# Kernel tuning notes

Measured on AMD Instinct MI355X. Metric: run time of the kernel, lower is better.

## Reference

```python
import jax, jax.numpy as jnp
import numpy as np

N_NODES = 50000
N_EDGES = 625000
F_IN = 128
HIDDEN = 128
N_CLASSES = 64


def setup_inputs() -> dict:
    key = jax.random.key(0)
    ks = jax.random.split(key, 8)
    x = jax.random.normal(ks[0], (N_NODES, F_IN), dtype=jnp.float32)
    edge_index = jax.random.randint(ks[1], (2, N_EDGES), 0, N_NODES, dtype=jnp.int64)
    # GCNConv weights (glorot-ish scale) and biases
    def glorot(k, fan_in, fan_out):
        s = jnp.sqrt(6.0 / (fan_in + fan_out))
        return jax.random.uniform(k, (fan_in, fan_out), minval=-s, maxval=s, dtype=jnp.float32)
    W1 = glorot(ks[2], F_IN, HIDDEN)
    b1 = jnp.zeros((HIDDEN,), dtype=jnp.float32)
    W2 = glorot(ks[3], HIDDEN, HIDDEN)
    b2 = jnp.zeros((HIDDEN,), dtype=jnp.float32)
    Wf = glorot(ks[4], HIDDEN, N_CLASSES)
    bf = jnp.zeros((N_CLASSES,), dtype=jnp.float32)
    return {"x": x, "edge_index": edge_index, "W1": W1, "b1": b1,
            "W2": W2, "b2": b2, "Wf": Wf, "bf": bf}


def reference(x, edge_index, W1, b1, W2, b2, Wf, bf):
    # Inference mode: AdaptiveDropout and F.dropout are identity (training=False).
    N = x.shape[0]
    loop = jnp.arange(N, dtype=edge_index.dtype)
    src = jnp.concatenate([edge_index[0], loop])  # source nodes (with self-loops)
    dst = jnp.concatenate([edge_index[1], loop])  # target nodes (with self-loops)
    # Symmetric GCN normalization: deg from edge weights scattered to targets
    deg = jax.ops.segment_sum(jnp.ones(dst.shape[0], dtype=x.dtype), dst, num_segments=N)
    dinv = jnp.where(deg > 0, jax.lax.rsqrt(deg), 0.0)
    norm = dinv[src] * dinv[dst]  # [E+N]

    def gcn(h, W, b):
        m = h @ W                      # [N, out]
        msg = m[src] * norm[:, None]   # gather + scale  [E+N, out]
        return jax.ops.segment_sum(msg, dst, num_segments=N) + b

    h = jax.nn.relu(gcn(x, W1, b1))
    h = jax.nn.relu(gcn(h, W2, b2))
    logits = gcn(h, Wf, bf)
    return jax.nn.log_softmax(logits, axis=1)
```

## Files before the change

### kernel.cpp

```cpp
#include <hip/hip_runtime.h>
#include <cstdint>
#include <cstddef>


#define WAVE 64
typedef _Float16 f16;
typedef f16  f16x2 __attribute__((ext_vector_type(2)));
typedef f16  f16x4 __attribute__((ext_vector_type(4)));
typedef f16  f16x8 __attribute__((ext_vector_type(8)));
typedef float f32x4 __attribute__((ext_vector_type(4)));


__global__ void k_zero(int4* __restrict__ p, int n4) {
    int i = blockIdx.x * blockDim.x + threadIdx.x;
    if (i < n4) p[i] = make_int4(0, 0, 0, 0);
}

__global__ void k_count(const int* __restrict__ dst, int E, int* __restrict__ cnt, int N) {
    int e = blockIdx.x * blockDim.x + threadIdx.x;
    if (e >= E) return;
    int d = dst[e];
    if (d >= 0 && d < N) atomicAdd(&cnt[d], 1);
}

__global__ __launch_bounds__(256) void k_blocksum(const int* __restrict__ cnt, int N,
                                                  int* __restrict__ partial) {
    const int t  = threadIdx.x;
    const int b  = blockIdx.x;
    const int i0 = b * 1024 + t * 4;
    int s = 0;
#pragma unroll
    for (int j = 0; j < 4; ++j) {
        int i = i0 + j;
        if (i < N) s += cnt[i];
    }
#pragma unroll
    for (int o = 32; o > 0; o >>= 1) s += __shfl_xor(s, o);
    __shared__ int ws[4];
    if ((t & 63) == 0) ws[t >> 6] = s;
    __syncthreads();
    if (t == 0) partial[b] = ws[0] + ws[1] + ws[2] + ws[3];
}

__global__ __launch_bounds__(256) void k_blockscan(const int* __restrict__ cnt, int N,
                                                   const int* __restrict__ partial, int numB,
                                                   int* __restrict__ offs,
                                                   float* __restrict__ dinv,
                                                   int* __restrict__ cursor) {
    const int t  = threadIdx.x;
    const int b  = blockIdx.x;
    const int i0 = b * 1024 + t * 4;
    __shared__ int sbase;
    __shared__ int ws[4];

    if (t < 64) {
        int v = 0;
        for (int i = t; i < b; i += 64) v += partial[i];
#pragma unroll
        for (int o = 32; o > 0; o >>= 1) v += __shfl_xor(v, o);
        if (t == 0) sbase = v;
    }

    int c[4];
    int tsum = 0;
#pragma unroll
    for (int j = 0; j < 4; ++j) {
        int i = i0 + j;
        c[j] = (i < N) ? cnt[i] : 0;
        tsum += c[j];
    }
    int incl = tsum;
#pragma unroll
    for (int o = 1; o < 64; o <<= 1) {
        int u = __shfl_up(incl, o);
        if ((t & 63) >= o) incl += u;
    }
    const int wid = t >> 6;
    if ((t & 63) == 63) ws[wid] = incl;
    __syncthreads();
    int wbase = 0;
    for (int w = 0; w < wid; ++w) wbase += ws[w];
    int run = sbase + wbase + (incl - tsum);
#pragma unroll
    for (int j = 0; j < 4; ++j) {
        int i = i0 + j;
        if (i < N) {
            offs[i]   = run;
            run      += c[j];
            dinv[i]   = rsqrtf((float)(c[j] + 1));
            cursor[i] = 0;
        }
    }
    if (b == numB - 1 && t == 0)
        offs[N] = sbase + ws[0] + ws[1] + ws[2] + ws[3];
}

__global__ void k_scatter(const int* __restrict__ src, const int* __restrict__ dst, int E,
                          const int* __restrict__ offsets, int* __restrict__ cursor,
                          int* __restrict__ src_s, int N) {
    int e = blockIdx.x * blockDim.x + threadIdx.x;
    if (e >= E) return;
    int d = dst[e], s = src[e];
    if (d < 0 || d >= N || s < 0 || s >= N) return;
    int p = offsets[d] + atomicAdd(&cursor[d], 1);
    src_s[p] = s;
}

__global__ void k_cvt_w_all(const float* __restrict__ W1, const float* __restrict__ W2,
                            const float* __restrict__ Wf,
                            f16* __restrict__ Wt1, f16* __restrict__ Wt2,
                            f16* __restrict__ Wtf) {
    int i = blockIdx.x * 256 + threadIdx.x;
    if (i < 16384) {
        int n = i >> 7, k = i & 127;
        Wt1[i] = (f16)W1[k * 128 + n];
    } else if (i < 32768) {
        int j = i - 16384;
        int n = j >> 7, k = j & 127;
        Wt2[j] = (f16)W2[k * 128 + n];
    } else if (i < 40960) {
        int j = i - 32768;
        int n = j >> 7, k = j & 127;
        Wtf[j] = (f16)Wf[k * 64 + n];
    }
}

template <int OUT, bool AF32>
__global__ __launch_bounds__(256) void k_gemm_mfma(const void* __restrict__ Av,
                                                   const f16* __restrict__ Wt,
                                                   const float* __restrict__ dinv,
                                                   f16* __restrict__ M,
                                                   int N) {
    constexpr int K  = 128;
    constexpr int CW = OUT / 64;
    __shared__ char smem[OUT * K * 2];
    __shared__ float dl[64];

    const int t    = threadIdx.x;
    const int w    = t >> 6;
    const int lane = t & 63;
    const int ln   = lane & 15;
    const int lh   = lane >> 4;
    const int row0 = blockIdx.x * 64;

    {
        constexpr int NCH = OUT * 16;
        for (int j = t; j < NCH; j += 256) {
            int n = j >> 4;
            uint32_t byte = (uint32_t)j * 16;
            uint32_t swz  = byte ^ (uint32_t)((n & 7) << 4);
            *(f16x8*)(smem + swz) = *(const f16x8*)&Wt[(size_t)j * 8];
        }
        if (t < 64) {
            int r = row0 + t;
            dl[t] = dinv[r < N ? r : (N - 1)];
        }
    }
    __syncthreads();

    f16x8 bfr[CW][4];
    const int c0 = w * CW;
#pragma unroll
    for (int c = 0; c < CW; ++c) {
        int n = (c0 + c) * 16 + ln;
#pragma unroll
        for (int q = 0; q < 4; ++q) {
            uint32_t byte = (uint32_t)(n * 256 + q * 64 + lh * 16);
            uint32_t swz  = byte ^ (uint32_t)((n & 7) << 4);
            bfr[c][q] = *(const f16x8*)(smem + swz);
        }
    }
    __syncthreads();

    f32x4 acc[4][CW];
#pragma unroll
    for (int s = 0; s < 4; ++s)
#pragma unroll
        for (int c = 0; c < CW; ++c)
            acc[s][c] = f32x4{0.f, 0.f, 0.f, 0.f};

#pragma unroll
    for (int s = 0; s < 4; ++s) {
        int m = row0 + s * 16 + ln;
        const size_t mrow = (size_t)(m < N ? m : (N - 1)) * K;
#pragma unroll
        for (int q = 0; q < 4; ++q) {
            f16x8 a;
            if constexpr (AF32) {
                const float* ap = (const float*)Av + mrow + q * 32 + lh * 8;
                float4 x0 = *(const float4*)ap;
                float4 x1 = *(const float4*)(ap + 4);
                a = f16x8{ (f16)x0.x, (f16)x0.y, (f16)x0.z, (f16)x0.w,
                           (f16)x1.x, (f16)x1.y, (f16)x1.z, (f16)x1.w };
            } else {
                a = *(const f16x8*)((const f16*)Av + mrow + q * 32 + lh * 8);
            }
#pragma unroll
            for (int c = 0; c < CW; ++c)
                acc[s][c] = __builtin_amdgcn_mfma_f32_16x16x32_f16(a, bfr[c][q], acc[s][c], 0, 0, 0);
        }
    }

    f16* ot = (f16*)smem;
#pragma unroll
    for (int s = 0; s < 4; ++s) {
#pragma unroll
        for (int c = 0; c < CW; ++c) {
            int col = (c0 + c) * 16 + ln;
#pragma unroll
            for (int r = 0; r < 4; ++r) {
                int rl = s * 16 + lh * 4 + r;
                ot[rl * OUT + col] = (f16)(acc[s][c][r] * dl[rl]);
            }
        }
    }
    __syncthreads();

    constexpr int CPR = OUT / 8;
    for (int j = t; j < 64 * CPR; j += 256) {
        int rl = j / CPR;
        if (row0 + rl < N)
            *(f16x8*)&M[(size_t)(row0 + rl) * OUT + (j % CPR) * 8] =
                *(const f16x8*)&ot[(size_t)j * 8];
    }
}

__global__ __launch_bounds__(256) void k_agg128_f16(const f16* __restrict__ M16,
                                                    const int* __restrict__ offs,
                                                    const int* __restrict__ srcs,
                                                    const float* __restrict__ dinv,
                                                    const float* __restrict__ bias,
                                                    f16* __restrict__ H16, int N) {
    const int lane = threadIdx.x & (WAVE - 1);
    const int sub  = lane >> 5;
    const int hl   = lane & 31;
    const int q    = hl >> 4;
    const int fl   = lane & 15;
    const int fo   = fl * 8;
    const int node = blockIdx.x * 8 + (threadIdx.x >> 6) * 2 + sub;
    if (node >= N) return;

    float a[8] = {0.f, 0.f, 0.f, 0.f, 0.f, 0.f, 0.f, 0.f};
    if (q == 0) {
        f16x8 v = *(const f16x8*)&M16[(size_t)node * 128 + fo];
#pragma unroll
        for (int i = 0; i < 8; ++i) a[i] = (float)v[i];
    }

    const int e0 = offs[node], e1 = offs[node + 1];
    for (int base = e0; base < e1; base += 16) {
        int   s[8];
        float w[8];
#pragma unroll
        for (int j = 0; j < 8; ++j) {
            int i = base + 2 * j + q;
            bool ok = i < e1;
            s[j] = srcs[ok ? i : e0];
            w[j] = ok ? 1.f : 0.f;
        }
        f16x8 v[8];
#pragma unroll
        for (int j = 0; j < 8; ++j)
            v[j] = *(const f16x8*)&M16[(size_t)s[j] * 128 + fo];
#pragma unroll
        for (int j = 0; j < 8; ++j)
#pragma unroll
            for (int i = 0; i < 8; ++i)
                a[i] += w[j] * (float)v[j][i];
    }

#pragma unroll
    for (int i = 0; i < 8; ++i) a[i] += __shfl_xor(a[i], 16);

    if (q == 0) {
        const float dn = dinv[node];
        float4 b0 = *(const float4*)&bias[fo];
        float4 b1 = *(const float4*)&bias[fo + 4];
        f16x8 o;
        o[0] = (f16)fmaxf(a[0] * dn + b0.x, 0.f);
        o[1] = (f16)fmaxf(a[1] * dn + b0.y, 0.f);
        o[2] = (f16)fmaxf(a[2] * dn + b0.z, 0.f);
        o[3] = (f16)fmaxf(a[3] * dn + b0.w, 0.f);
        o[4] = (f16)fmaxf(a[4] * dn + b1.x, 0.f);
        o[5] = (f16)fmaxf(a[5] * dn + b1.y, 0.f);
        o[6] = (f16)fmaxf(a[6] * dn + b1.z, 0.f);
        o[7] = (f16)fmaxf(a[7] * dn + b1.w, 0.f);
        *(f16x8*)&H16[(size_t)node * 128 + fo] = o;
    }
}

__global__ __launch_bounds__(256) void k_agg64_lsm(const f16* __restrict__ M16,
                                                   const int* __restrict__ offs,
                                                   const int* __restrict__ srcs,
                                                   const float* __restrict__ dinv,
                                                   const float* __restrict__ bias,
                                                   float* __restrict__ Y, int N) {
    const int lane = threadIdx.x & (WAVE - 1);
    const int sub  = lane >> 5;
    const int hl   = lane & 31;
    const int q    = hl >> 4;
    const int fl   = lane & 15;
    const int fo   = fl * 4;
    const int node = blockIdx.x * 8 + (threadIdx.x >> 6) * 2 + sub;
    if (node >= N) return;

    float a[4] = {0.f, 0.f, 0.f, 0.f};
    if (q == 0) {
        f16x4 v = *(const f16x4*)&M16[(size_t)node * 64 + fo];
#pragma unroll
        for (int i = 0; i < 4; ++i) a[i] = (float)v[i];
    }

    const int e0 = offs[node], e1 = offs[node + 1];
    for (int base = e0; base < e1; base += 16) {
        int   s[8];
        float w[8];
#pragma unroll
        for (int j = 0; j < 8; ++j) {
            int i = base + 2 * j + q;
            bool ok = i < e1;
            s[j] = srcs[ok ? i : e0];
            w[j] = ok ? 1.f : 0.f;
        }
        f16x4 v[8];
#pragma unroll
        for (int j = 0; j < 8; ++j)
            v[j] = *(const f16x4*)&M16[(size_t)s[j] * 64 + fo];
#pragma unroll
        for (int j = 0; j < 8; ++j)
#pragma unroll
            for (int i = 0; i < 4; ++i)
                a[i] += w[j] * (float)v[j][i];
    }

#pragma unroll
    for (int i = 0; i < 4; ++i) a[i] += __shfl_xor(a[i], 16);

    const float dn = dinv[node];
    float4 b = *(const float4*)&bias[fo];
    float v0 = a[0] * dn + b.x;
    float v1 = a[1] * dn + b.y;
    float v2 = a[2] * dn + b.z;
    float v3 = a[3] * dn + b.w;
    float m = fmaxf(fmaxf(v0, v1), fmaxf(v2, v3));
#pragma unroll
    for (int o = 8; o > 0; o >>= 1) m = fmaxf(m, __shfl_xor(m, o));
    float s = expf(v0 - m) + expf(v1 - m) + expf(v2 - m) + expf(v3 - m);
#pragma unroll
    for (int o = 8; o > 0; o >>= 1) s += __shfl_xor(s, o);
    if (q == 0) {
        float ls = logf(s);
        float4 o4 = make_float4(v0 - m - ls, v1 - m - ls, v2 - m - ls, v3 - m - ls);
        *(float4*)&Y[(size_t)node * 64 + fo] = o4;
    }
}


extern "C" void kernel_launch(void* const* d_in, const int* in_sizes, int n_in,
                              void* d_out, int out_size, void* d_ws, size_t ws_size,
                              hipStream_t stream) {
    const float* x  = (const float*)d_in[0];
    const int*   ei = (const int*)d_in[1];
    const float* W1 = (const float*)d_in[2];
    const float* b1 = (const float*)d_in[3];
    const float* W2 = (const float*)d_in[4];
    const float* b2 = (const float*)d_in[5];
    const float* Wf = (const float*)d_in[6];
    const float* bf = (const float*)d_in[7];
    float* out = (float*)d_out;

    const int N = in_sizes[0] / 128;
    const int E = in_sizes[1] / 2;
    const int* src = ei;
    const int* dst = ei + E;

    char* ws = (char*)d_ws;
    auto alloc = [&](size_t bytes) -> void* {
        void* p = ws;
        ws += (bytes + 255) & ~(size_t)255;
        return p;
    };
    const int numB = (N + 1023) / 1024;
    int*   cnt    = (int*)alloc((size_t)N * 4);
    int*   cursor = (int*)alloc((size_t)N * 4);
    int*   offs   = (int*)alloc((size_t)(N + 1) * 4);
    float* dinv   = (float*)alloc((size_t)N * 4);
    int*   part   = (int*)alloc((size_t)numB * 4);
    int*   src_s  = (int*)alloc((size_t)E * 4);
    f16*   m16    = (f16*)alloc((size_t)N * 128 * 2);
    f16*   h16    = (f16*)alloc((size_t)N * 128 * 2);
    f16*   Wt1    = (f16*)alloc(128 * 128 * 2);
    f16*   Wt2    = (f16*)alloc(128 * 128 * 2);
    f16*   Wtf    = (f16*)alloc(128 * 64 * 2);

    const int TB = 256;
    const int n4 = (N + 3) / 4;
    k_zero<<<(n4 + TB - 1) / TB, TB, 0, stream>>>((int4*)cnt, n4);
    k_count<<<(E + TB - 1) / TB, TB, 0, stream>>>(dst, E, cnt, N);
    k_blocksum<<<numB, 256, 0, stream>>>(cnt, N, part);
    k_blockscan<<<numB, 256, 0, stream>>>(cnt, N, part, numB, offs, dinv, cursor);
    k_scatter<<<(E + TB - 1) / TB, TB, 0, stream>>>(src, dst, E, offs, cursor, src_s, N);
    k_cvt_w_all<<<160, 256, 0, stream>>>(W1, W2, Wf, Wt1, Wt2, Wtf);

    const int gemm_grid = (N + 63) / 64;
    const int agg_grid  = (N + 7) / 8;

    k_gemm_mfma<128, true><<<gemm_grid, 256, 0, stream>>>(x, Wt1, dinv, m16, N);
    k_agg128_f16<<<agg_grid, 256, 0, stream>>>(m16, offs, src_s, dinv, b1, h16, N);

    k_gemm_mfma<128, false><<<gemm_grid, 256, 0, stream>>>(h16, Wt2, dinv, m16, N);
    k_agg128_f16<<<agg_grid, 256, 0, stream>>>(m16, offs, src_s, dinv, b2, h16, N);

    k_gemm_mfma<64, false><<<gemm_grid, 256, 0, stream>>>(h16, Wtf, dinv, m16, N);
    k_agg64_lsm<<<agg_grid, 256, 0, stream>>>(m16, offs, src_s, dinv, bf, out, N);
}
```

Before: 201.2 us.

## Fuse whole GCN pipeline into one cooperative persistent kernel with grid syncs

Replaces the twelve separate launches (CSR build, weight conversion, three GEMM and aggregation pairs) with a single cooperative persistent kernel that loops over tiles and separates phases with grid.sync(). It also overlaps the edge scatter with the first GEMM in the same phase. The aim is to remove per-launch overhead and tail gaps between small kernels. In exchange, occupancy is capped by the cooperative-launch limit and the 32KB static shared memory, and every grid barrier stalls the whole device. The old multi-kernel path stays as a fallback if the cooperative launch fails.

```diff
diff --git a/kernel.cpp b/kernel.cpp
--- a/kernel.cpp
+++ b/kernel.cpp
@@ -1,6 +1,9 @@
 #include <hip/hip_runtime.h>
+#include <hip/hip_cooperative_groups.h>
 #include <cstdint>
 #include <cstddef>
+
+namespace cg = cooperative_groups;
 
 
 #define WAVE 64
@@ -11,106 +14,10 @@
 typedef float f32x4 __attribute__((ext_vector_type(4)));
 
 
-__global__ void k_zero(int4* __restrict__ p, int n4) {
-    int i = blockIdx.x * blockDim.x + threadIdx.x;
-    if (i < n4) p[i] = make_int4(0, 0, 0, 0);
-}
-
-__global__ void k_count(const int* __restrict__ dst, int E, int* __restrict__ cnt, int N) {
-    int e = blockIdx.x * blockDim.x + threadIdx.x;
-    if (e >= E) return;
-    int d = dst[e];
-    if (d >= 0 && d < N) atomicAdd(&cnt[d], 1);
-}
-
-__global__ __launch_bounds__(256) void k_blocksum(const int* __restrict__ cnt, int N,
-                                                  int* __restrict__ partial) {
-    const int t  = threadIdx.x;
-    const int b  = blockIdx.x;
-    const int i0 = b * 1024 + t * 4;
-    int s = 0;
-#pragma unroll
-    for (int j = 0; j < 4; ++j) {
-        int i = i0 + j;
-        if (i < N) s += cnt[i];
-    }
-#pragma unroll
-    for (int o = 32; o > 0; o >>= 1) s += __shfl_xor(s, o);
-    __shared__ int ws[4];
-    if ((t & 63) == 0) ws[t >> 6] = s;
-    __syncthreads();
-    if (t == 0) partial[b] = ws[0] + ws[1] + ws[2] + ws[3];
-}
-
-__global__ __launch_bounds__(256) void k_blockscan(const int* __restrict__ cnt, int N,
-                                                   const int* __restrict__ partial, int numB,
-                                                   int* __restrict__ offs,
-                                                   float* __restrict__ dinv,
-                                                   int* __restrict__ cursor) {
-    const int t  = threadIdx.x;
-    const int b  = blockIdx.x;
-    const int i0 = b * 1024 + t * 4;
-    __shared__ int sbase;
-    __shared__ int ws[4];
-
-    if (t < 64) {
-        int v = 0;
-        for (int i = t; i < b; i += 64) v += partial[i];
-#pragma unroll
-        for (int o = 32; o > 0; o >>= 1) v += __shfl_xor(v, o);
-        if (t == 0) sbase = v;
-    }
-
-    int c[4];
-    int tsum = 0;
-#pragma unroll
-    for (int j = 0; j < 4; ++j) {
-        int i = i0 + j;
-        c[j] = (i < N) ? cnt[i] : 0;
-        tsum += c[j];
-    }
-    int incl = tsum;
-#pragma unroll
-    for (int o = 1; o < 64; o <<= 1) {
-        int u = __shfl_up(incl, o);
-        if ((t & 63) >= o) incl += u;
-    }
-    const int wid = t >> 6;
-    if ((t & 63) == 63) ws[wid] = incl;
-    __syncthreads();
-    int wbase = 0;
-    for (int w = 0; w < wid; ++w) wbase += ws[w];
-    int run = sbase + wbase + (incl - tsum);
-#pragma unroll
-    for (int j = 0; j < 4; ++j) {
-        int i = i0 + j;
-        if (i < N) {
-            offs[i]   = run;
-            run      += c[j];
-            dinv[i]   = rsqrtf((float)(c[j] + 1));
-            cursor[i] = 0;
-        }
-    }
-    if (b == numB - 1 && t == 0)
-        offs[N] = sbase + ws[0] + ws[1] + ws[2] + ws[3];
-}
-
-__global__ void k_scatter(const int* __restrict__ src, const int* __restrict__ dst, int E,
-                          const int* __restrict__ offsets, int* __restrict__ cursor,
-                          int* __restrict__ src_s, int N) {
-    int e = blockIdx.x * blockDim.x + threadIdx.x;
-    if (e >= E) return;
-    int d = dst[e], s = src[e];
-    if (d < 0 || d >= N || s < 0 || s >= N) return;
-    int p = offsets[d] + atomicAdd(&cursor[d], 1);
-    src_s[p] = s;
-}
-
-__global__ void k_cvt_w_all(const float* __restrict__ W1, const float* __restrict__ W2,
-                            const float* __restrict__ Wf,
-                            f16* __restrict__ Wt1, f16* __restrict__ Wt2,
-                            f16* __restrict__ Wtf) {
-    int i = blockIdx.x * 256 + threadIdx.x;
+__device__ __forceinline__ void cvtw_elem(int i,
+    const float* __restrict__ W1, const float* __restrict__ W2,
+    const float* __restrict__ Wf,
+    f16* __restrict__ Wt1, f16* __restrict__ Wt2, f16* __restrict__ Wtf) {
     if (i < 16384) {
         int n = i >> 7, k = i & 127;
         Wt1[i] = (f16)W1[k * 128 + n];
@@ -125,23 +32,86 @@
     }
 }
 
+__device__ __forceinline__ void blocksum_body(const int* __restrict__ cnt, int N,
+                                              int* __restrict__ part, int b, int t,
+                                              int* ws4) {
+    const int i0 = b * 1024 + t * 4;
+    int s = 0;
+#pragma unroll
+    for (int j = 0; j < 4; ++j) {
+        int i = i0 + j;
+        if (i < N) s += cnt[i];
+    }
+#pragma unroll
+    for (int o = 32; o > 0; o >>= 1) s += __shfl_xor(s, o);
+    if ((t & 63) == 0) ws4[t >> 6] = s;
+    __syncthreads();
+    if (t == 0) part[b] = ws4[0] + ws4[1] + ws4[2] + ws4[3];
+    __syncthreads();
+}
+
+__device__ __forceinline__ void blockscan_body(const int* __restrict__ cnt, int N,
+                                               const int* __restrict__ part, int numB,
+                                               int* __restrict__ offs,
+                                               float* __restrict__ dinv,
+                                               int* __restrict__ cursor,
+                                               int b, int t, int* ws4, int* sbase) {
+    const int i0 = b * 1024 + t * 4;
+    if (t < 64) {
+        int v = 0;
+        for (int i = t; i < b; i += 64) v += part[i];
+#pragma unroll
+        for (int o = 32; o > 0; o >>= 1) v += __shfl_xor(v, o);
+        if (t == 0) *sbase = v;
+    }
+    int c[4];
+    int tsum = 0;
+#pragma unroll
+    for (int j = 0; j < 4; ++j) {
+        int i = i0 + j;
+        c[j] = (i < N) ? cnt[i] : 0;
+        tsum += c[j];
+    }
+    int incl = tsum;
+#pragma unroll
+    for (int o = 1; o < 64; o <<= 1) {
+        int u = __shfl_up(incl, o);
+        if ((t & 63) >= o) incl += u;
+    }
+    const int wid = t >> 6;
+    if ((t & 63) == 63) ws4[wid] = incl;
+    __syncthreads();
+    int wbase = 0;
+    for (int w = 0; w < wid; ++w) wbase += ws4[w];
+    int run = *sbase + wbase + (incl - tsum);
+#pragma unroll
+    for (int j = 0; j < 4; ++j) {
+        int i = i0 + j;
+        if (i < N) {
+            offs[i]   = run;
+            run      += c[j];
+            dinv[i]   = rsqrtf((float)(c[j] + 1));
+            cursor[i] = 0;
+        }
+    }
+    if (b == numB - 1 && t == 0)
+        offs[N] = *sbase + ws4[0] + ws4[1] + ws4[2] + ws4[3];
+    __syncthreads();
+}
+
 template <int OUT, bool AF32>
-__global__ __launch_bounds__(256) void k_gemm_mfma(const void* __restrict__ Av,
-                                                   const f16* __restrict__ Wt,
-                                                   const float* __restrict__ dinv,
-                                                   f16* __restrict__ M,
-                                                   int N) {
+__device__ __forceinline__ void gemm_tile(const void* __restrict__ Av,
+                                          const f16* __restrict__ Wt,
+                                          const float* __restrict__ dinv,
+                                          f16* __restrict__ M, int N, int row0,
+                                          char* smem, float* dl) {
     constexpr int K  = 128;
     constexpr int CW = OUT / 64;
-    __shared__ char smem[OUT * K * 2];
-    __shared__ float dl[64];
-
     const int t    = threadIdx.x;
     const int w    = t >> 6;
     const int lane = t & 63;
     const int ln   = lane & 15;
     const int lh   = lane >> 4;
-    const int row0 = blockIdx.x * 64;
 
     {
         constexpr int NCH = OUT * 16;
@@ -223,21 +193,22 @@
             *(f16x8*)&M[(size_t)(row0 + rl) * OUT + (j % CPR) * 8] =
                 *(const f16x8*)&ot[(size_t)j * 8];
     }
-}
-
-__global__ __launch_bounds__(256) void k_agg128_f16(const f16* __restrict__ M16,
-                                                    const int* __restrict__ offs,
-                                                    const int* __restrict__ srcs,
-                                                    const float* __restrict__ dinv,
-                                                    const float* __restrict__ bias,
-                                                    f16* __restrict__ H16, int N) {
-    const int lane = threadIdx.x & (WAVE - 1);
+    __syncthreads();
+}
+
+__device__ __forceinline__ void agg128_tile(const f16* __restrict__ M16,
+                                            const int* __restrict__ offs,
+                                            const int* __restrict__ srcs,
+                                            const float* __restrict__ dinv,
+                                            const float* __restrict__ bias,
+                                            f16* __restrict__ H16, int N, int vb) {
+    const int t    = threadIdx.x;
+    const int lane = t & (WAVE - 1);
     const int sub  = lane >> 5;
-    const int hl   = lane & 31;
-    const int q    = hl >> 4;
+    const int q    = (lane & 31) >> 4;
     const int fl   = lane & 15;
     const int fo   = fl * 8;
-    const int node = blockIdx.x * 8 + (threadIdx.x >> 6) * 2 + sub;
+    const int node = vb * 8 + (t >> 6) * 2 + sub;
     if (node >= N) return;
 
     float a[8] = {0.f, 0.f, 0.f, 0.f, 0.f, 0.f, 0.f, 0.f};
@@ -289,19 +260,19 @@
     }
 }
 
-__global__ __launch_bounds__(256) void k_agg64_lsm(const f16* __restrict__ M16,
-                                                   const int* __restrict__ offs,
-                                                   const int* __restrict__ srcs,
-                                                   const float* __restrict__ dinv,
-                                                   const float* __restrict__ bias,
-                                                   float* __restrict__ Y, int N) {
-    const int lane = threadIdx.x & (WAVE - 1);
+__device__ __forceinline__ void agg64_tile(const f16* __restrict__ M16,
+                                           const int* __restrict__ offs,
+                                           const int* __restrict__ srcs,
+                                           const float* __restrict__ dinv,
+                                           const float* __restrict__ bias,
+                                           float* __restrict__ Y, int N, int vb) {
+    const int t    = threadIdx.x;
+    const int lane = t & (WAVE - 1);
     const int sub  = lane >> 5;
-    const int hl   = lane & 31;
-    const int q    = hl >> 4;
+    const int q    = (lane & 31) >> 4;
     const int fl   = lane & 15;
     const int fo   = fl * 4;
-    const int node = blockIdx.x * 8 + (threadIdx.x >> 6) * 2 + sub;
+    const int node = vb * 8 + (t >> 6) * 2 + sub;
     if (node >= N) return;
 
     float a[4] = {0.f, 0.f, 0.f, 0.f};
@@ -353,6 +324,173 @@
         float4 o4 = make_float4(v0 - m - ls, v1 - m - ls, v2 - m - ls, v3 - m - ls);
         *(float4*)&Y[(size_t)node * 64 + fo] = o4;
     }
+}
+
+
+__global__ __launch_bounds__(256, 4) void k_mega(
+    const float* __restrict__ x, const int* __restrict__ srcv, const int* __restrict__ dstv,
+    const float* __restrict__ W1, const float* __restrict__ b1,
+    const float* __restrict__ W2, const float* __restrict__ b2,
+    const float* __restrict__ Wf, const float* __restrict__ bf,
+    float* __restrict__ out,
+    int* cnt, int* cursor, int* offs, float* dinv, int* part, int* src_s,
+    f16* m16, f16* h16, f16* Wt1, f16* Wt2, f16* Wtf,
+    int N, int E, int numB) {
+    cg::grid_group grid = cg::this_grid();
+    __shared__ char  smem[32768];
+    __shared__ float dl[64];
+    __shared__ int   ws4[4];
+    __shared__ int   sbase;
+
+    const int t    = threadIdx.x;
+    const int gtid = blockIdx.x * 256 + t;
+    const int gsz  = gridDim.x * 256;
+
+    {
+        const int n4 = (N + 3) >> 2;
+        const int4 z = make_int4(0, 0, 0, 0);
+        for (int i = gtid; i < n4; i += gsz) ((int4*)cnt)[i] = z;
+        for (int i = gtid; i < 40960; i += gsz) cvtw_elem(i, W1, W2, Wf, Wt1, Wt2, Wtf);
+    }
+    grid.sync();
+
+    for (int e = gtid; e < E; e += gsz) {
+        int d = dstv[e];
+        if ((unsigned)d < (unsigned)N) atomicAdd(&cnt[d], 1);
+    }
+    grid.sync();
+
+    for (int b = blockIdx.x; b < numB; b += gridDim.x)
+        blocksum_body(cnt, N, part, b, t, ws4);
+    grid.sync();
+
+    for (int b = blockIdx.x; b < numB; b += gridDim.x)
+        blockscan_body(cnt, N, part, numB, offs, dinv, cursor, b, t, ws4, &sbase);
+    grid.sync();
+
+    for (int e = gtid; e < E; e += gsz) {
+        int d = dstv[e], s = srcv[e];
+        if ((unsigned)d < (unsigned)N && (unsigned)s < (unsigned)N) {
+            int p = offs[d] + atomicAdd(&cursor[d], 1);
+            src_s[p] = s;
+        }
+    }
+    {
+        const int tiles = (N + 63) >> 6;
+        for (int vt = blockIdx.x; vt < tiles; vt += gridDim.x)
+            gemm_tile<128, true>(x, Wt1, dinv, m16, N, vt * 64, smem, dl);
+    }
+    grid.sync();
+
+    {
+        const int vbs = (N + 7) >> 3;
+        for (int vb = blockIdx.x; vb < vbs; vb += gridDim.x)
+            agg128_tile(m16, offs, src_s, dinv, b1, h16, N, vb);
+    }
+    grid.sync();
+
+    {
+        const int tiles = (N + 63) >> 6;
+        for (int vt = blockIdx.x; vt < tiles; vt += gridDim.x)
+            gemm_tile<128, false>(h16, Wt2, dinv, m16, N, vt * 64, smem, dl);
+    }
+    grid.sync();
+
+    {
+        const int vbs = (N + 7) >> 3;
+        for (int vb = blockIdx.x; vb < vbs; vb += gridDim.x)
+            agg128_tile(m16, offs, src_s, dinv, b2, h16, N, vb);
+    }
+    grid.sync();
+
+    {
+        const int tiles = (N + 63) >> 6;
+        for (int vt = blockIdx.x; vt < tiles; vt += gridDim.x)
+            gemm_tile<64, false>(h16, Wtf, dinv, m16, N, vt * 64, smem, dl);
+    }
+    grid.sync();
+
+    {
+        const int vbs = (N + 7) >> 3;
+        for (int vb = blockIdx.x; vb < vbs; vb += gridDim.x)
+            agg64_tile(m16, offs, src_s, dinv, bf, out, N, vb);
+    }
+}
+
+
+__global__ void k_zero(int4* __restrict__ p, int n4) {
+    int i = blockIdx.x * blockDim.x + threadIdx.x;
+    if (i < n4) p[i] = make_int4(0, 0, 0, 0);
+}
+
+__global__ void k_count(const int* __restrict__ dst, int E, int* __restrict__ cnt, int N) {
+    int e = blockIdx.x * blockDim.x + threadIdx.x;
+    if (e >= E) return;
+    int d = dst[e];
+    if ((unsigned)d < (unsigned)N) atomicAdd(&cnt[d], 1);
+}
+
+__global__ __launch_bounds__(256) void k_blocksum(const int* __restrict__ cnt, int N,
+                                                  int* __restrict__ part) {
+    __shared__ int ws4[4];
+    blocksum_body(cnt, N, part, blockIdx.x, threadIdx.x, ws4);
+}
+
+__global__ __launch_bounds__(256) void k_blockscan(const int* __restrict__ cnt, int N,
+                                                   const int* __restrict__ part, int numB,
+                                                   int* __restrict__ offs,
+                                                   float* __restrict__ dinv,
+                                                   int* __restrict__ cursor) {
+    __shared__ int ws4[4];
+    __shared__ int sbase;
+    blockscan_body(cnt, N, part, numB, offs, dinv, cursor, blockIdx.x, threadIdx.x, ws4, &sbase);
+}
+
+__global__ void k_scatter(const int* __restrict__ src, const int* __restrict__ dst, int E,
+                          const int* __restrict__ offsets, int* __restrict__ cursor,
+                          int* __restrict__ src_s, int N) {
+    int e = blockIdx.x * blockDim.x + threadIdx.x;
+    if (e >= E) return;
+    int d = dst[e], s = src[e];
+    if ((unsigned)d >= (unsigned)N || (unsigned)s >= (unsigned)N) return;
+    int p = offsets[d] + atomicAdd(&cursor[d], 1);
+    src_s[p] = s;
+}
+
+__global__ void k_cvt_w_all(const float* __restrict__ W1, const float* __restrict__ W2,
+                            const float* __restrict__ Wf,
+                            f16* __restrict__ Wt1, f16* __restrict__ Wt2,
+                            f16* __restrict__ Wtf) {
+    int i = blockIdx.x * 256 + threadIdx.x;
+    cvtw_elem(i, W1, W2, Wf, Wt1, Wt2, Wtf);
+}
+
+template <int OUT, bool AF32>
+__global__ __launch_bounds__(256) void k_gemm_mfma(const void* __restrict__ Av,
+                                                   const f16* __restrict__ Wt,
+                                                   const float* __restrict__ dinv,
+                                                   f16* __restrict__ M, int N) {
+    __shared__ char  smem[OUT * 128 * 2];
+    __shared__ float dl[64];
+    gemm_tile<OUT, AF32>(Av, Wt, dinv, M, N, blockIdx.x * 64, smem, dl);
+}
+
+__global__ __launch_bounds__(256) void k_agg128_f16(const f16* __restrict__ M16,
+                                                    const int* __restrict__ offs,
+                                                    const int* __restrict__ srcs,
+                                                    const float* __restrict__ dinv,
+                                                    const float* __restrict__ bias,
+                                                    f16* __restrict__ H16, int N) {
+    agg128_tile(M16, offs, srcs, dinv, bias, H16, N, blockIdx.x);
+}
+
+__global__ __launch_bounds__(256) void k_agg64_lsm(const f16* __restrict__ M16,
+                                                   const int* __restrict__ offs,
+                                                   const int* __restrict__ srcs,
+                                                   const float* __restrict__ dinv,
+                                                   const float* __restrict__ bias,
+                                                   float* __restrict__ Y, int N) {
+    agg64_tile(M16, offs, srcs, dinv, bias, Y, N, blockIdx.x);
 }
 
 
@@ -371,8 +509,8 @@
 
     const int N = in_sizes[0] / 128;
     const int E = in_sizes[1] / 2;
-    const int* src = ei;
-    const int* dst = ei + E;
+    const int* srcv = ei;
+    const int* dstv = ei + E;
 
     char* ws = (char*)d_ws;
     auto alloc = [&](size_t bytes) -> void* {
@@ -381,7 +519,7 @@
         return p;
     };
     const int numB = (N + 1023) / 1024;
-    int*   cnt    = (int*)alloc((size_t)N * 4);
+    int*   cnt    = (int*)alloc((size_t)N * 4 + 16);
     int*   cursor = (int*)alloc((size_t)N * 4);
     int*   offs   = (int*)alloc((size_t)(N + 1) * 4);
     float* dinv   = (float*)alloc((size_t)N * 4);
@@ -393,13 +531,36 @@
     f16*   Wt2    = (f16*)alloc(128 * 128 * 2);
     f16*   Wtf    = (f16*)alloc(128 * 64 * 2);
 
+    int dev = 0;
+    hipGetDevice(&dev);
+    int nCU = 256;
+    hipDeviceGetAttribute(&nCU, hipDeviceAttributeMultiprocessorCount, dev);
+    int occ = 0;
+    hipError_t oe = hipOccupancyMaxActiveBlocksPerMultiprocessor(&occ, (const void*)k_mega, 256, 0);
+    if (oe != hipSuccess || occ < 1) occ = 1;
+    if (occ > 8) occ = 8;
+    int grid = nCU * occ;
+
+    int Nv = N, Ev = E, numBv = numB;
+    void* args[] = {
+        (void*)&x, (void*)&srcv, (void*)&dstv,
+        (void*)&W1, (void*)&b1, (void*)&W2, (void*)&b2, (void*)&Wf, (void*)&bf,
+        (void*)&out,
+        (void*)&cnt, (void*)&cursor, (void*)&offs, (void*)&dinv, (void*)&part, (void*)&src_s,
+        (void*)&m16, (void*)&h16, (void*)&Wt1, (void*)&Wt2, (void*)&Wtf,
+        (void*)&Nv, (void*)&Ev, (void*)&numBv,
+    };
+    hipError_t ce = hipLaunchCooperativeKernel((void*)k_mega, dim3(grid), dim3(256),
+                                               args, 0, stream);
+    if (ce == hipSuccess) return;
+
     const int TB = 256;
     const int n4 = (N + 3) / 4;
     k_zero<<<(n4 + TB - 1) / TB, TB, 0, stream>>>((int4*)cnt, n4);
-    k_count<<<(E + TB - 1) / TB, TB, 0, stream>>>(dst, E, cnt, N);
+    k_count<<<(E + TB - 1) / TB, TB, 0, stream>>>(dstv, E, cnt, N);
     k_blocksum<<<numB, 256, 0, stream>>>(cnt, N, part);
     k_blockscan<<<numB, 256, 0, stream>>>(cnt, N, part, numB, offs, dinv, cursor);
-    k_scatter<<<(E + TB - 1) / TB, TB, 0, stream>>>(src, dst, E, offs, cursor, src_s, N);
+    k_scatter<<<(E + TB - 1) / TB, TB, 0, stream>>>(srcv, dstv, E, offs, cursor, src_s, N);
     k_cvt_w_all<<<160, 256, 0, stream>>>(W1, W2, Wf, Wt1, Wt2, Wtf);
 
     const int gemm_grid = (N + 63) / 64;
```

After: 745.0 us. 3.7x slower.
